# Kernel tuning notes

Hardware: AMD Instinct MI355X
Metric: run time of the kernel (lower is better)

Reference implementation:

```python
import jax, jax.numpy as jnp
import numpy as np

B, D_IN, T, H = 256, 22, 1000, 64
G = 4 * H  # 256 gate rows, PyTorch order i,f,g,o


def _lstm_dir(x, w_ih, w_hh, b_ih, b_hh, reverse):
    # x: (B,T,D); w_ih: (4H,D); w_hh: (4H,H)
    xw = jnp.einsum('btd,gd->btg', x, w_ih) + b_ih + b_hh  # (B,T,4H)
    h0 = jnp.zeros((x.shape[0], H), x.dtype)

    def step(carry, xw_t):
        h, c = carry
        gates = xw_t + h @ w_hh.T
        i, f, g, o = jnp.split(gates, 4, axis=-1)
        i = jax.nn.sigmoid(i)
        f = jax.nn.sigmoid(f)
        g = jnp.tanh(g)
        o = jax.nn.sigmoid(o)
        c = f * c + i * g
        h = o * jnp.tanh(c)
        return (h, c), h

    _, hs = jax.lax.scan(step, (h0, h0), jnp.swapaxes(xw, 0, 1), reverse=reverse)
    return jnp.swapaxes(hs, 0, 1)  # (B,T,H), index t aligned with input t


def _bilstm_layer(x, w_ih, w_hh, b_ih, b_hh):
    hf = _lstm_dir(x, w_ih[0], w_hh[0], b_ih[0], b_hh[0], False)
    hb = _lstm_dir(x, w_ih[1], w_hh[1], b_ih[1], b_hh[1], True)
    return jnp.concatenate([hf, hb], axis=-1)  # (B,T,2H)


def setup_inputs() -> dict:
    key = jax.random.key(0)
    ks = jax.random.split(key, 8)
    s = 0.1  # keep gates out of deep saturation
    return {
        'x': jax.random.normal(ks[0], (B, D_IN, T), jnp.float32),
        'w_ih_first': jax.random.normal(ks[1], (2, G, D_IN), jnp.float32) * s,
        'w_ih_rest': jax.random.normal(ks[2], (3, 2, G, 2 * H), jnp.float32) * s,
        'w_hh': jax.random.normal(ks[3], (4, 2, G, H), jnp.float32) * s,
        'b_ih': jax.random.normal(ks[4], (4, 2, G), jnp.float32) * s,
        'b_hh': jax.random.normal(ks[5], (4, 2, G), jnp.float32) * s,
        'w_lin': jax.random.normal(ks[6], (54, 2 * H), jnp.float32) * s,
        'b_lin': jax.random.normal(ks[7], (54,), jnp.float32) * s,
    }


def reference(x, w_ih_first, w_ih_rest, w_hh, b_ih, b_hh, w_lin, b_lin):
    # x: (B, 22, T) -> (B, T, 22) as in torch .transpose(1, 2)
    out = jnp.swapaxes(x, 1, 2)
    # 4 stacked bidirectional layers: lstm1.l0, lstm1.l1, lstm2.l0, lstm2.l1
    out = _bilstm_layer(out, w_ih_first, w_hh[0], b_ih[0], b_hh[0])
    for i in range(3):
        out = _bilstm_layer(out, w_ih_rest[i], w_hh[i + 1], b_ih[i + 1], b_hh[i + 1])
    # last timestep -> linear head (B, 54)
    return out[:, -1, :] @ w_lin.T + b_lin
```

## Files before the change

### kernel.cpp

```cpp
#include <hip/hip_runtime.h>
#include <hip/hip_bf16.h>
#include <type_traits>

#define T_    1000
#define NB    256
#define HH    64
#define GG    256

typedef float f32x4 __attribute__((ext_vector_type(4)));
typedef __bf16 bf16x8 __attribute__((ext_vector_type(8)));

__device__ __forceinline__ void barrier_lds() {
    asm volatile("s_waitcnt lgkmcnt(0)\n\ts_barrier" ::: "memory");
}

__device__ __forceinline__ float fast_sigmoid(float x) {
    float e = __expf(-x);
    return __builtin_amdgcn_rcpf(1.f + e);
}
__device__ __forceinline__ float fast_tanh(float x) {
    x = fmaxf(x, -15.f);
    float e = __expf(-2.f * x);
    return (1.f - e) * __builtin_amdgcn_rcpf(1.f + e);
}
__device__ __forceinline__ float bf2f(unsigned short u) {
    return __builtin_bit_cast(float, (unsigned)u << 16);
}

__global__ void prep_w(const float* __restrict__ wihf, const float* __restrict__ wihr,
                       const float* __restrict__ whh, const float* __restrict__ bih,
                       const float* __restrict__ bhh,
                       __bf16* __restrict__ w0H, __bf16* __restrict__ w0L,
                       __bf16* __restrict__ wrH, __bf16* __restrict__ whH,
                       float* __restrict__ bias, float* __restrict__ w0f) {
    int i = blockIdx.x * 256 + threadIdx.x;
    if (i < 2 * GG * 32) {
        int k = i & 31, gd = i >> 5;
        float w = (k < 22) ? wihf[gd * 22 + k] : 0.f;
        __bf16 h = (__bf16)w;
        w0H[i] = h; w0L[i] = (__bf16)(w - (float)h);
        w0f[i] = w;
    }
    if (i < 3 * 2 * GG * 128) wrH[i] = (__bf16)wihr[i];
    if (i < 4 * 2 * GG * HH)  whH[i] = (__bf16)whh[i];
    if (i < 4 * 2 * GG)       bias[i] = bih[i] + bhh[i];
}

__global__ __launch_bounds__(256) void prep_x_ps(const float* __restrict__ x,
                                                 __bf16* __restrict__ xhi,
                                                 __bf16* __restrict__ xlo) {
    const int b = blockIdx.x;
    __shared__ float xs[22][104];
    for (int tc = 0; tc < 10; ++tc) {
        const int t0 = tc * 100;
        __syncthreads();
        for (int i = threadIdx.x; i < 22 * 100; i += 256) {
            int k = i / 100, t = i - k * 100;
            xs[k][t] = x[((size_t)b * 22 + k) * T_ + t0 + t];
        }
        __syncthreads();
        for (int i = threadIdx.x; i < 100 * 4; i += 256) {
            int t = i >> 2, p = i & 3;
            bf16x8 vh, vl;
            #pragma unroll
            for (int j = 0; j < 8; ++j) {
                int k = p * 8 + j;
                float f = (k < 22) ? xs[k][t] : 0.f;
                __bf16 h = (__bf16)f;
                vh[j] = h;
                vl[j] = (__bf16)(f - (float)h);
            }
            *(bf16x8*)(xhi + ((size_t)b * T_ + t0 + t) * 32 + p * 8) = vh;
            *(bf16x8*)(xlo + ((size_t)b * T_ + t0 + t) * 32 + p * 8) = vl;
        }
    }
}

__global__ __launch_bounds__(256) void prep_x_b(const float* __restrict__ x,
                                                __bf16* __restrict__ xp) {
    const int b = blockIdx.x;
    __shared__ float xs[22][104];
    for (int tc = 0; tc < 10; ++tc) {
        const int t0 = tc * 100;
        __syncthreads();
        for (int i = threadIdx.x; i < 22 * 100; i += 256) {
            int k = i / 100, t = i - k * 100;
            xs[k][t] = x[((size_t)b * 22 + k) * T_ + t0 + t];
        }
        __syncthreads();
        for (int i = threadIdx.x; i < 100 * 4; i += 256) {
            int t = i >> 2, p = i & 3;
            bf16x8 v;
            #pragma unroll
            for (int j = 0; j < 8; ++j) {
                int k = p * 8 + j;
                v[j] = (k < 22) ? (__bf16)xs[k][t] : (__bf16)0.f;
            }
            *(bf16x8*)(xp + ((size_t)b * T_ + t0 + t) * 32 + p * 8) = v;
        }
    }
}

template<int KCH, bool L0, bool FIN>
__global__ __launch_bounds__(256, 1) void fused_scan3(
    const __bf16* __restrict__ inA,
    const __bf16* __restrict__ inB,
    const __bf16* __restrict__ wihH,
    const __bf16* __restrict__ wihL,
    const __bf16* __restrict__ whhH,
    const float*  __restrict__ bias,
    __bf16* __restrict__ out,
    float* __restrict__ outF)
{
    const int dir = blockIdx.y;
    const int b0 = blockIdx.x * 2;
    const int tid = threadIdx.x;
    const int wv = tid >> 6, lane = tid & 63;
    const int j2 = lane & 15, q = lane >> 4;
    const int ch_l = j2 >> 3;
    const int u_l = j2 & 7;
    constexpr int KIN = KCH * 32;

    __shared__ __align__(16) __bf16 hbuf[2][2][80];
    __shared__ float cbuf[2][72];

    bf16x8 wf[4][KCH], wfl[4][L0 ? KCH : 1];
    bf16x8 whf[4][2];
    float bgate[4];
    #pragma unroll
    for (int F = 0; F < 4; ++F) {
        const int g = (F * 4 + wv) * 16 + j2;
        bgate[F] = bias[dir * GG + g];
        #pragma unroll
        for (int ks = 0; ks < KCH; ++ks) {
            wf[F][ks] = *(const bf16x8*)(wihH + ((size_t)dir * GG + g) * KIN + ks * 32 + q * 8);
            if constexpr (L0)
                wfl[F][ks] = *(const bf16x8*)(wihL + ((size_t)dir * GG + g) * KIN + ks * 32 + q * 8);
        }
        #pragma unroll
        for (int ks = 0; ks < 2; ++ks)
            whf[F][ks] = *(const bf16x8*)(whhH + ((size_t)dir * GG + g) * HH + ks * 32 + q * 8);
    }
    if (tid < 64) {
        cbuf[0][tid] = 0.f; cbuf[1][tid] = 0.f;
        hbuf[1][0][tid] = (__bf16)0.f;
        hbuf[1][1][tid] = (__bf16)0.f;
    }
    __syncthreads();

    bf16x8 xfh[KCH], xfl[L0 ? KCH : 1];
    auto issue_x = [&](int grp) {
        int s = grp * 8 + u_l;
        if (s > T_ - 1) s = T_ - 1;
        int tt = dir ? (T_ - 1) - s : s;
        const __bf16* ph = inA + ((size_t)(b0 + ch_l) * T_ + tt) * KIN + q * 8;
        #pragma unroll
        for (int ks = 0; ks < KCH; ++ks)
            xfh[ks] = *(const bf16x8*)(ph + ks * 32);
        if constexpr (L0) {
            const __bf16* pl = inB + ((size_t)(b0 + ch_l) * T_ + tt) * KIN + q * 8;
            #pragma unroll
            for (int ks = 0; ks < KCH; ++ks)
                xfl[ks] = *(const bf16x8*)(pl + ks * 32);
        }
    };

    f32x4 Pu[4], Pn[4];
    #pragma unroll
    for (int F = 0; F < 4; ++F) { Pu[F] = (f32x4){0.f,0.f,0.f,0.f}; Pn[F] = (f32x4){0.f,0.f,0.f,0.f}; }
    issue_x(0);
    #pragma unroll
    for (int ks = 0; ks < KCH; ++ks)
        #pragma unroll
        for (int F = 0; F < 4; ++F)
            Pu[F] = __builtin_amdgcn_mfma_f32_16x16x32_bf16(xfh[ks], wf[F][ks], Pu[F], 0, 0, 0);
    if constexpr (L0) {
        #pragma unroll
        for (int ks = 0; ks < KCH; ++ks)
            #pragma unroll
            for (int F = 0; F < 4; ++F)
                Pu[F] = __builtin_amdgcn_mfma_f32_16x16x32_bf16(xfl[ks], wf[F][ks], Pu[F], 0, 0, 0);
        #pragma unroll
        for (int ks = 0; ks < KCH; ++ks)
            #pragma unroll
            for (int F = 0; F < 4; ++F)
                Pu[F] = __builtin_amdgcn_mfma_f32_16x16x32_bf16(xfh[ks], wfl[F][ks], Pu[F], 0, 0, 0);
    }
    #pragma unroll
    for (int F = 0; F < 4; ++F)
        #pragma unroll
        for (int r4 = 0; r4 < 4; ++r4)
            Pu[F][r4] += bgate[F];
    issue_x(1);

    float hsave[8];
    float creg = 0.f;

    for (int grp = 0; grp < 125; ++grp) {
        #pragma unroll
        for (int u = 0; u < 8; ++u) {
            const int s = grp * 8 + u;
            const int rp = (s + 1) & 1;
            bf16x8 ah0 = *(const bf16x8*)&hbuf[rp][ch_l][q * 8];
            bf16x8 ah1 = *(const bf16x8*)&hbuf[rp][ch_l][32 + q * 8];

            if constexpr (!L0) {
                const int ks = u >> 1;
                const int Fb = (u & 1) * 2;
                Pn[Fb]     = __builtin_amdgcn_mfma_f32_16x16x32_bf16(xfh[ks], wf[Fb][ks],     Pn[Fb], 0, 0, 0);
                Pn[Fb + 1] = __builtin_amdgcn_mfma_f32_16x16x32_bf16(xfh[ks], wf[Fb + 1][ks], Pn[Fb + 1], 0, 0, 0);
            } else {
                if (u == 0) {
                    #pragma unroll
                    for (int F = 0; F < 4; ++F)
                        Pn[F] = __builtin_amdgcn_mfma_f32_16x16x32_bf16(xfh[0], wf[F][0], Pn[F], 0, 0, 0);
                } else if (u == 1) {
                    #pragma unroll
                    for (int F = 0; F < 4; ++F)
                        Pn[F] = __builtin_amdgcn_mfma_f32_16x16x32_bf16(xfl[0], wf[F][0], Pn[F], 0, 0, 0);
                } else if (u == 2) {
                    #pragma unroll
                    for (int F = 0; F < 4; ++F)
                        Pn[F] = __builtin_amdgcn_mfma_f32_16x16x32_bf16(xfh[0], wfl[F][0], Pn[F], 0, 0, 0);
                }
            }

            f32x4 R[4];
            #pragma unroll
            for (int F = 0; F < 4; ++F) R[F] = (f32x4){0.f, 0.f, 0.f, 0.f};
            #pragma unroll
            for (int F = 0; F < 4; ++F)
                R[F] = __builtin_amdgcn_mfma_f32_16x16x32_bf16(ah0, whf[F][0], R[F], 0, 0, 0);
            #pragma unroll
            for (int F = 0; F < 4; ++F)
                R[F] = __builtin_amdgcn_mfma_f32_16x16x32_bf16(ah1, whf[F][1], R[F], 0, 0, 0);

            const int r = u & 3;
            const int ch = q >> 1;
            const bool owner = ((q & 1) == (u >> 2));
            float cold = (u == 0 || u == 4) ? cbuf[ch][wv * 16 + j2] : creg;
            float iv = Pu[0][r] + R[0][r];
            float fv = Pu[1][r] + R[1][r];
            float gv = Pu[2][r] + R[2][r];
            float ov = Pu[3][r] + R[3][r];
            float cn = fast_sigmoid(fv) * cold + fast_sigmoid(iv) * fast_tanh(gv);
            float hn = fast_sigmoid(ov) * fast_tanh(cn);
            creg = cn;
            if (owner) {
                if (u == 3 || u == 7) cbuf[ch][wv * 16 + j2] = cn;
                hbuf[s & 1][ch][wv * 16 + j2] = (__bf16)hn;
                hsave[u] = hn;
            }
            if (u == 7) issue_x(grp + 2);
            barrier_lds();
        }
        #pragma unroll
        for (int u = 0; u < 8; ++u) {
            if ((q & 1) == (u >> 2)) {
                const int s = grp * 8 + u;
                const int tt = dir ? (T_ - 1) - s : s;
                const size_t col = dir * HH + wv * 16 + j2;
                out[((size_t)(b0 + (q >> 1)) * T_ + tt) * 128 + col] = (__bf16)hsave[u];
                if constexpr (FIN)
                    if (tt == T_ - 1)
                        outF[(size_t)(b0 + (q >> 1)) * 128 + col] = hsave[u];
            }
        }
        #pragma unroll
        for (int F = 0; F < 4; ++F) {
            Pu[F] = Pn[F];
            Pn[F] = (f32x4){0.f, 0.f, 0.f, 0.f};
            #pragma unroll
            for (int r4 = 0; r4 < 4; ++r4) Pu[F][r4] += bgate[F];
        }
    }
}

template<int KIN, typename TI, typename TO>
__global__ __launch_bounds__(256, 2) void scan_valu(
    const TI* __restrict__ in, const float* __restrict__ wih,
    const float* __restrict__ whh, const float* __restrict__ bias,
    TO* __restrict__ out)
{
    const int dir = blockIdx.y, bb = blockIdx.x, g = threadIdx.x;
    __shared__ __align__(16) float xs[8][KIN];
    __shared__ __align__(16) float act[256];
    __shared__ __align__(16) float hs[2][64];

    float wk[KIN], wr[64];
    {
        const float* wp = wih + (size_t)(dir * GG + g) * KIN;
        #pragma unroll
        for (int k4 = 0; k4 < KIN / 4; ++k4) {
            f32x4 v = *(const f32x4*)(wp + k4 * 4);
            wk[k4 * 4 + 0] = v.x; wk[k4 * 4 + 1] = v.y;
            wk[k4 * 4 + 2] = v.z; wk[k4 * 4 + 3] = v.w;
        }
        const float* rp = whh + (size_t)(dir * GG + g) * HH;
        #pragma unroll
        for (int j4 = 0; j4 < 16; ++j4) {
            f32x4 v = *(const f32x4*)(rp + j4 * 4);
            wr[j4 * 4 + 0] = v.x; wr[j4 * 4 + 1] = v.y;
            wr[j4 * 4 + 2] = v.z; wr[j4 * 4 + 3] = v.w;
        }
    }
    const float bg = bias[dir * GG + g];
    const bool is_g = (g >= 128 && g < 192);
    float c = 0.f;
    if (g < 64) hs[0][g] = 0.f;
    __syncthreads();

    float hreg[8];
    for (int ch = 0; ch < 125; ++ch) {
        if constexpr (KIN == 128) {
            int l = g * 4, u = l >> 7, k = l & 127;
            int s = ch * 8 + u, tt = dir ? (T_ - 1) - s : s;
            const TI* src = in + ((size_t)bb * T_ + tt) * 128 + k;
            f32x4 fv;
            if constexpr (std::is_same_v<TI, float>) fv = *(const f32x4*)src;
            else {
                ushort4 rv = *(const ushort4*)src;
                fv = (f32x4){bf2f(rv.x), bf2f(rv.y), bf2f(rv.z), bf2f(rv.w)};
            }
            *(f32x4*)&xs[u][k] = fv;
        } else {
            int u = g >> 5, k = g & 31;
            int s = ch * 8 + u, tt = dir ? (T_ - 1) - s : s;
            if constexpr (std::is_same_v<TI, float>)
                xs[u][k] = in[((size_t)bb * T_ + tt) * 32 + k];
            else
                xs[u][k] = bf2f(((const unsigned short*)in)[((size_t)bb * T_ + tt) * 32 + k]);
        }
        __syncthreads();
        #pragma unroll
        for (int u = 0; u < 8; ++u) {
            const int p = (ch * 8 + u) & 1;
            float a0 = bg, a1 = 0.f, a2 = 0.f, a3 = 0.f;
            #pragma unroll
            for (int k = 0; k < KIN; k += 4) {
                f32x4 xv = *(const f32x4*)&xs[u][k];
                a0 = fmaf(xv.x, wk[k + 0], a0); a1 = fmaf(xv.y, wk[k + 1], a1);
                a2 = fmaf(xv.z, wk[k + 2], a2); a3 = fmaf(xv.w, wk[k + 3], a3);
            }
            #pragma unroll
            for (int j = 0; j < 64; j += 4) {
                f32x4 hv = *(const f32x4*)&hs[p][j];
                a0 = fmaf(hv.x, wr[j + 0], a0); a1 = fmaf(hv.y, wr[j + 1], a1);
                a2 = fmaf(hv.z, wr[j + 2], a2); a3 = fmaf(hv.w, wr[j + 3], a3);
            }
            float a = (a0 + a1) + (a2 + a3);
            act[g] = is_g ? fast_tanh(a) : fast_sigmoid(a);
            __syncthreads();
            if (g < 64) {
                float iv = act[g], fv = act[64 + g], gv = act[128 + g], ov = act[192 + g];
                c = fmaf(fv, c, iv * gv);
                float hn = ov * fast_tanh(c);
                hs[p ^ 1][g] = hn;
                hreg[u] = hn;
            }
            __syncthreads();
        }
        if (g < 64) {
            #pragma unroll
            for (int u = 0; u < 8; ++u) {
                int s = ch * 8 + u, tt = dir ? (T_ - 1) - s : s;
                out[((size_t)bb * T_ + tt) * 128 + dir * HH + g] = (TO)hreg[u];
            }
        }
    }
}

__global__ __launch_bounds__(64) void head_last(
    const float* __restrict__ hl, const float* __restrict__ wlin,
    const float* __restrict__ blin, float* __restrict__ outp) {
    const int b = blockIdx.x, tid = threadIdx.x;
    __shared__ float hv[128];
    hv[tid] = hl[(size_t)b * 128 + tid];
    hv[64 + tid] = hl[(size_t)b * 128 + 64 + tid];
    __syncthreads();
    if (tid < 54) {
        float a = blin[tid];
        #pragma unroll 4
        for (int j = 0; j < 128; ++j) a = fmaf(hv[j], wlin[tid * 128 + j], a);
        outp[b * 54 + tid] = a;
    }
}

template<typename TI>
__global__ __launch_bounds__(64) void head_kernel(
    const TI* __restrict__ fin, const float* __restrict__ wlin,
    const float* __restrict__ blin, float* __restrict__ outp) {
    const int b = blockIdx.x, tid = threadIdx.x;
    __shared__ float hv[128];
    #pragma unroll
    for (int rr = 0; rr < 2; ++rr) {
        int j = rr * 64 + tid;
        hv[j] = (float)fin[((size_t)b * T_ + (T_ - 1)) * 128 + j];
    }
    __syncthreads();
    if (tid < 54) {
        float a = blin[tid];
        #pragma unroll 4
        for (int j = 0; j < 128; ++j) a = fmaf(hv[j], wlin[tid * 128 + j], a);
        outp[b * 54 + tid] = a;
    }
}

extern "C" void kernel_launch(void* const* d_in, const int* in_sizes, int n_in,
                              void* d_out, int out_size, void* d_ws, size_t ws_size,
                              hipStream_t stream) {
    const float* x    = (const float*)d_in[0];
    const float* wihf = (const float*)d_in[1];
    const float* wihr = (const float*)d_in[2];
    const float* whh  = (const float*)d_in[3];
    const float* bih  = (const float*)d_in[4];
    const float* bhh  = (const float*)d_in[5];
    const float* wlin = (const float*)d_in[6];
    const float* blin = (const float*)d_in[7];
    float* outp = (float*)d_out;

    char* ws = (char*)d_ws;
    const size_t PB = (size_t)NB * T_ * 128 * sizeof(__bf16);
    const size_t PX = (size_t)NB * T_ * 32 * sizeof(__bf16);
    const size_t HL = (size_t)NB * 128 * sizeof(float);
    const size_t WSZ = 794624;
    const bool primary = ws_size >= 2 * PB + 2 * PX + HL + WSZ;

    char* sw = primary ? (ws + 2 * PB + 2 * PX + HL) : (ws + 2 * PB);
    __bf16* w0H  = (__bf16*)(sw);
    __bf16* w0L  = (__bf16*)(sw + 32768);
    __bf16* wrH  = (__bf16*)(sw + 65536);
    __bf16* whH  = (__bf16*)(sw + 458752);
    float*  bias = (float*) (sw + 720896);
    float*  w0f  = (float*) (sw + 729088);

    prep_w<<<768, 256, 0, stream>>>(wihf, wihr, whh, bih, bhh,
                                    w0H, w0L, wrH, whH, bias, w0f);

    if (primary) {
        __bf16* A   = (__bf16*)ws;
        __bf16* B   = (__bf16*)(ws + PB);
        __bf16* xhi = (__bf16*)(ws + 2 * PB);
        __bf16* xlo = (__bf16*)(ws + 2 * PB + PX);
        float*  hl  = (float*)(ws + 2 * PB + 2 * PX);
        prep_x_ps<<<NB, 256, 0, stream>>>(x, xhi, xlo);
        const dim3 sgrid(NB / 2, 2);
        fused_scan3<1, true,  false><<<sgrid, 256, 0, stream>>>(xhi, xlo, w0H, w0L, whH, bias, A, nullptr);
        fused_scan3<4, false, false><<<sgrid, 256, 0, stream>>>(A, nullptr, wrH, nullptr,
            whH + 32768, bias + 512, B, nullptr);
        fused_scan3<4, false, false><<<sgrid, 256, 0, stream>>>(B, nullptr, wrH + 65536, nullptr,
            whH + 65536, bias + 1024, A, nullptr);
        fused_scan3<4, false, true><<<sgrid, 256, 0, stream>>>(A, nullptr, wrH + 131072, nullptr,
            whH + 98304, bias + 1536, B, hl);
        head_last<<<NB, 64, 0, stream>>>(hl, wlin, blin, outp);
    } else {
        __bf16* A = (__bf16*)ws;
        __bf16* B = (__bf16*)(ws + PB);
        __bf16* xp = (__bf16*)ws;
        prep_x_b<<<NB, 256, 0, stream>>>(x, xp);
        const dim3 vgrid(NB, 2);
        scan_valu<32, __bf16, __bf16><<<vgrid, 256, 0, stream>>>(xp, w0f, whh, bias, B);
        scan_valu<128, __bf16, __bf16><<<vgrid, 256, 0, stream>>>(B, wihr,          whh + 32768, bias + 512,  A);
        scan_valu<128, __bf16, __bf16><<<vgrid, 256, 0, stream>>>(A, wihr + 65536,  whh + 65536, bias + 1024, B);
        scan_valu<128, __bf16, __bf16><<<vgrid, 256, 0, stream>>>(B, wihr + 131072, whh + 98304, bias + 1536, A);
        head_kernel<__bf16><<<NB, 64, 0, stream>>>(A, wlin, blin, outp);
    }
}
```

Before: 1.354 ms.

## Double-buffer x prefetch, defer output flush, and pass cell state via lane swizzle

Input fragments are now double-buffered across two register sets. The next group's load is issued at the first step of a group rather than the last, and the group loop is unrolled by two to alternate buffers. The cell-state handoff between lane halves now uses a ds_swizzle cross-lane exchange instead of an LDS buffer. The previous group's hidden-state stores are deferred into the first step of the next group, and the recurrent MFMA chains are reordered per gate. The aim is to hide global-load and store latency and to take LDS traffic off the serial recurrence, at the cost of more registers and more complex control flow.

```diff
diff --git a/kernel.cpp b/kernel.cpp
--- a/kernel.cpp
+++ b/kernel.cpp
@@ -122,7 +122,8 @@
     constexpr int KIN = KCH * 32;
 
     __shared__ __align__(16) __bf16 hbuf[2][2][80];
-    __shared__ float cbuf[2][72];
+
+    const f32x4 Z4 = (f32x4){0.f, 0.f, 0.f, 0.f};
 
     bf16x8 wf[4][KCH], wfl[4][L0 ? KCH : 1];
     bf16x8 whf[4][2];
@@ -142,138 +143,157 @@
             whf[F][ks] = *(const bf16x8*)(whhH + ((size_t)dir * GG + g) * HH + ks * 32 + q * 8);
     }
     if (tid < 64) {
-        cbuf[0][tid] = 0.f; cbuf[1][tid] = 0.f;
         hbuf[1][0][tid] = (__bf16)0.f;
         hbuf[1][1][tid] = (__bf16)0.f;
     }
     __syncthreads();
 
-    bf16x8 xfh[KCH], xfl[L0 ? KCH : 1];
-    auto issue_x = [&](int grp) {
+    bf16x8 xfA[KCH], xfB[KCH];
+    bf16x8 xlA[L0 ? KCH : 1], xlB[L0 ? KCH : 1];
+    auto issue_x = [&](int grp, auto& dh, auto& dl) {
         int s = grp * 8 + u_l;
         if (s > T_ - 1) s = T_ - 1;
         int tt = dir ? (T_ - 1) - s : s;
         const __bf16* ph = inA + ((size_t)(b0 + ch_l) * T_ + tt) * KIN + q * 8;
         #pragma unroll
         for (int ks = 0; ks < KCH; ++ks)
-            xfh[ks] = *(const bf16x8*)(ph + ks * 32);
+            dh[ks] = *(const bf16x8*)(ph + ks * 32);
         if constexpr (L0) {
             const __bf16* pl = inB + ((size_t)(b0 + ch_l) * T_ + tt) * KIN + q * 8;
             #pragma unroll
             for (int ks = 0; ks < KCH; ++ks)
-                xfl[ks] = *(const bf16x8*)(pl + ks * 32);
+                dl[ks] = *(const bf16x8*)(pl + ks * 32);
         }
     };
 
     f32x4 Pu[4], Pn[4];
     #pragma unroll
-    for (int F = 0; F < 4; ++F) { Pu[F] = (f32x4){0.f,0.f,0.f,0.f}; Pn[F] = (f32x4){0.f,0.f,0.f,0.f}; }
-    issue_x(0);
+    for (int F = 0; F < 4; ++F) { Pu[F] = Z4; Pn[F] = Z4; }
+    issue_x(0, xfA, xlA);
     #pragma unroll
     for (int ks = 0; ks < KCH; ++ks)
         #pragma unroll
         for (int F = 0; F < 4; ++F)
-            Pu[F] = __builtin_amdgcn_mfma_f32_16x16x32_bf16(xfh[ks], wf[F][ks], Pu[F], 0, 0, 0);
+            Pu[F] = __builtin_amdgcn_mfma_f32_16x16x32_bf16(xfA[ks], wf[F][ks], Pu[F], 0, 0, 0);
     if constexpr (L0) {
         #pragma unroll
         for (int ks = 0; ks < KCH; ++ks)
             #pragma unroll
             for (int F = 0; F < 4; ++F)
-                Pu[F] = __builtin_amdgcn_mfma_f32_16x16x32_bf16(xfl[ks], wf[F][ks], Pu[F], 0, 0, 0);
+                Pu[F] = __builtin_amdgcn_mfma_f32_16x16x32_bf16(xlA[ks], wf[F][ks], Pu[F], 0, 0, 0);
         #pragma unroll
         for (int ks = 0; ks < KCH; ++ks)
             #pragma unroll
             for (int F = 0; F < 4; ++F)
-                Pu[F] = __builtin_amdgcn_mfma_f32_16x16x32_bf16(xfh[ks], wfl[F][ks], Pu[F], 0, 0, 0);
+                Pu[F] = __builtin_amdgcn_mfma_f32_16x16x32_bf16(xfA[ks], wfl[F][ks], Pu[F], 0, 0, 0);
     }
     #pragma unroll
     for (int F = 0; F < 4; ++F)
         #pragma unroll
         for (int r4 = 0; r4 < 4; ++r4)
             Pu[F][r4] += bgate[F];
-    issue_x(1);
+    issue_x(1, xfB, xlB);
 
     float hsave[8];
     float creg = 0.f;
 
-    for (int grp = 0; grp < 125; ++grp) {
+    auto FLUSH = [&](int g) {
+        const int ch = q >> 1;
+        const size_t col = (size_t)dir * HH + wv * 16 + j2;
+        if (dir == 0) {
+            __bf16* base = out + ((size_t)(b0 + ch) * T_ + g * 8) * 128 + col;
+            #pragma unroll
+            for (int u = 0; u < 8; ++u)
+                if ((q & 1) == (u >> 2)) base[u * 128] = (__bf16)hsave[u];
+            if constexpr (FIN)
+                if (g == 124 && (q & 1) == 1)
+                    outF[(size_t)(b0 + ch) * 128 + col] = hsave[7];
+        } else {
+            __bf16* base = out + ((size_t)(b0 + ch) * T_ + ((T_ - 1) - g * 8)) * 128 + col;
+            #pragma unroll
+            for (int u = 0; u < 8; ++u)
+                if ((q & 1) == (u >> 2)) *(base - u * 128) = (__bf16)hsave[u];
+            if constexpr (FIN)
+                if (g == 0 && (q & 1) == 0)
+                    outF[(size_t)(b0 + ch) * 128 + col] = hsave[0];
+        }
+    };
+
+    auto GROUP = [&](int grp, auto& xcH, auto& xnH, auto& xcL, auto& xnL) {
         #pragma unroll
         for (int u = 0; u < 8; ++u) {
-            const int s = grp * 8 + u;
-            const int rp = (s + 1) & 1;
+            const int rp = (u + 1) & 1;
             bf16x8 ah0 = *(const bf16x8*)&hbuf[rp][ch_l][q * 8];
             bf16x8 ah1 = *(const bf16x8*)&hbuf[rp][ch_l][32 + q * 8];
+
+            if (u == 0 && grp > 0) FLUSH(grp - 1);
 
             if constexpr (!L0) {
                 const int ks = u >> 1;
                 const int Fb = (u & 1) * 2;
-                Pn[Fb]     = __builtin_amdgcn_mfma_f32_16x16x32_bf16(xfh[ks], wf[Fb][ks],     Pn[Fb], 0, 0, 0);
-                Pn[Fb + 1] = __builtin_amdgcn_mfma_f32_16x16x32_bf16(xfh[ks], wf[Fb + 1][ks], Pn[Fb + 1], 0, 0, 0);
+                Pn[Fb]     = __builtin_amdgcn_mfma_f32_16x16x32_bf16(xcH[ks], wf[Fb][ks],     Pn[Fb], 0, 0, 0);
+                Pn[Fb + 1] = __builtin_amdgcn_mfma_f32_16x16x32_bf16(xcH[ks], wf[Fb + 1][ks], Pn[Fb + 1], 0, 0, 0);
             } else {
                 if (u == 0) {
                     #pragma unroll
                     for (int F = 0; F < 4; ++F)
-                        Pn[F] = __builtin_amdgcn_mfma_f32_16x16x32_bf16(xfh[0], wf[F][0], Pn[F], 0, 0, 0);
+                        Pn[F] = __builtin_amdgcn_mfma_f32_16x16x32_bf16(xcH[0], wf[F][0], Pn[F], 0, 0, 0);
                 } else if (u == 1) {
                     #pragma unroll
                     for (int F = 0; F < 4; ++F)
-                        Pn[F] = __builtin_amdgcn_mfma_f32_16x16x32_bf16(xfl[0], wf[F][0], Pn[F], 0, 0, 0);
+                        Pn[F] = __builtin_amdgcn_mfma_f32_16x16x32_bf16(xcL[0], wf[F][0], Pn[F], 0, 0, 0);
                 } else if (u == 2) {
                     #pragma unroll
                     for (int F = 0; F < 4; ++F)
-                        Pn[F] = __builtin_amdgcn_mfma_f32_16x16x32_bf16(xfh[0], wfl[F][0], Pn[F], 0, 0, 0);
+                        Pn[F] = __builtin_amdgcn_mfma_f32_16x16x32_bf16(xcH[0], wfl[F][0], Pn[F], 0, 0, 0);
                 }
             }
 
             f32x4 R[4];
             #pragma unroll
-            for (int F = 0; F < 4; ++F) R[F] = (f32x4){0.f, 0.f, 0.f, 0.f};
-            #pragma unroll
-            for (int F = 0; F < 4; ++F)
-                R[F] = __builtin_amdgcn_mfma_f32_16x16x32_bf16(ah0, whf[F][0], R[F], 0, 0, 0);
-            #pragma unroll
-            for (int F = 0; F < 4; ++F)
-                R[F] = __builtin_amdgcn_mfma_f32_16x16x32_bf16(ah1, whf[F][1], R[F], 0, 0, 0);
+            for (int F = 0; F < 4; ++F) {
+                f32x4 t = __builtin_amdgcn_mfma_f32_16x16x32_bf16(ah0, whf[F][0], Z4, 0, 0, 0);
+                R[F] = __builtin_amdgcn_mfma_f32_16x16x32_bf16(ah1, whf[F][1], t, 0, 0, 0);
+            }
+
+            if (u == 0) issue_x(grp + 2, xnH, xnL);
 
             const int r = u & 3;
             const int ch = q >> 1;
-            const bool owner = ((q & 1) == (u >> 2));
-            float cold = (u == 0 || u == 4) ? cbuf[ch][wv * 16 + j2] : creg;
+            float cold = creg;
             float iv = Pu[0][r] + R[0][r];
             float fv = Pu[1][r] + R[1][r];
             float gv = Pu[2][r] + R[2][r];
             float ov = Pu[3][r] + R[3][r];
             float cn = fast_sigmoid(fv) * cold + fast_sigmoid(iv) * fast_tanh(gv);
             float hn = fast_sigmoid(ov) * fast_tanh(cn);
-            creg = cn;
+            if (u == 3 || u == 7)
+                creg = __builtin_bit_cast(float,
+                        __builtin_amdgcn_ds_swizzle(__builtin_bit_cast(int, cn), 0x401F));
+            else
+                creg = cn;
+            const bool owner = ((q & 1) == (u >> 2));
             if (owner) {
-                if (u == 3 || u == 7) cbuf[ch][wv * 16 + j2] = cn;
-                hbuf[s & 1][ch][wv * 16 + j2] = (__bf16)hn;
+                hbuf[u & 1][ch][wv * 16 + j2] = (__bf16)hn;
                 hsave[u] = hn;
             }
-            if (u == 7) issue_x(grp + 2);
             barrier_lds();
-        }
-        #pragma unroll
-        for (int u = 0; u < 8; ++u) {
-            if ((q & 1) == (u >> 2)) {
-                const int s = grp * 8 + u;
-                const int tt = dir ? (T_ - 1) - s : s;
-                const size_t col = dir * HH + wv * 16 + j2;
-                out[((size_t)(b0 + (q >> 1)) * T_ + tt) * 128 + col] = (__bf16)hsave[u];
-                if constexpr (FIN)
-                    if (tt == T_ - 1)
-                        outF[(size_t)(b0 + (q >> 1)) * 128 + col] = hsave[u];
-            }
         }
         #pragma unroll
         for (int F = 0; F < 4; ++F) {
             Pu[F] = Pn[F];
-            Pn[F] = (f32x4){0.f, 0.f, 0.f, 0.f};
+            Pn[F] = Z4;
             #pragma unroll
             for (int r4 = 0; r4 < 4; ++r4) Pu[F][r4] += bgate[F];
         }
-    }
+    };
+
+    for (int g2 = 0; g2 < 62; ++g2) {
+        GROUP(g2 * 2,     xfB, xfA, xlB, xlA);
+        GROUP(g2 * 2 + 1, xfA, xfB, xlA, xlB);
+    }
+    GROUP(124, xfB, xfA, xlB, xlA);
+    FLUSH(124);
 }
 
 template<int KIN, typename TI, typename TO>
```

Measured after the change: 1.182 ms, median of 2. -12.7%, faster.
